# Performance work log

Hardware: AMD Instinct MI355X
Metric: run time of the kernel (lower is better)

## Reference

```python
import jax, jax.numpy as jnp
import numpy as np

N, E, F_IN = 50000, 1600000, 256
H, C = 4, 32            # heads, hidden_channels
HC = H * C
NUM_CLASSES = 16
NUM_GRAPHS = 64
NEG_SLOPE = 0.2


def setup_inputs() -> dict:
    key = jax.random.key(0)
    ks = jax.random.split(key, 16)
    x = jax.random.normal(ks[0], (N, F_IN), dtype=jnp.float32)
    edge_index = jax.random.randint(ks[1], (2, E), 0, N, dtype=jnp.int32)
    batch = jnp.sort(jax.random.randint(ks[2], (N,), 0, NUM_GRAPHS, dtype=jnp.int32))
    def glorot(k, shape):
        fan = shape[0] + shape[-1]
        return jax.random.uniform(k, shape, jnp.float32, -1.0, 1.0) * np.sqrt(6.0 / fan)
    return {
        "x": x, "edge_index": edge_index, "batch": batch,
        # GATConv 1
        "W1": glorot(ks[3], (F_IN, HC)),
        "att_src1": glorot(ks[4], (H, C)),
        "att_dst1": glorot(ks[5], (H, C)),
        "b1": jnp.zeros((HC,), jnp.float32),
        # GATConv 2
        "W2": glorot(ks[6], (HC, HC)),
        "att_src2": glorot(ks[7], (H, C)),
        "att_dst2": glorot(ks[8], (H, C)),
        "b2": jnp.zeros((HC,), jnp.float32),
        # classifier
        "Wc1": glorot(ks[9], (HC, C)),
        "bc1": jnp.zeros((C,), jnp.float32),
        "Wc2": glorot(ks[10], (C, NUM_CLASSES)),
        "bc2": jnp.zeros((NUM_CLASSES,), jnp.float32),
    }


def _gat_conv(x, src, dst, W, a_src, a_dst, b):
    # x: [N, F_in] -> h: [N, H, C]
    h = (x @ W).reshape(N, H, C)
    alpha_src = jnp.sum(h * a_src, axis=-1)   # [N, H]
    alpha_dst = jnp.sum(h * a_dst, axis=-1)   # [N, H]
    e = alpha_src[src] + alpha_dst[dst]       # [Etot, H]
    e = jax.nn.leaky_relu(e, NEG_SLOPE)
    # segment softmax over incoming edges of each dst node
    m = jax.ops.segment_max(e, dst, num_segments=N)          # [N, H]
    p = jnp.exp(e - m[dst])                                  # [Etot, H]
    z = jax.ops.segment_sum(p, dst, num_segments=N)          # [N, H]
    w = p / z[dst]
    out = jax.ops.segment_sum(h[src] * w[:, :, None], dst, num_segments=N)
    return out.reshape(N, HC) + b


def reference(x, edge_index, batch, W1, att_src1, att_dst1, b1,
              W2, att_src2, att_dst2, b2, Wc1, bc1, Wc2, bc2):
    # PyG GATConv default: add self-loops
    loop = jnp.arange(N, dtype=edge_index.dtype)
    src = jnp.concatenate([edge_index[0], loop])
    dst = jnp.concatenate([edge_index[1], loop])

    h = _gat_conv(x, src, dst, W1, att_src1, att_dst1, b1)
    h = jax.nn.relu(h)
    h = _gat_conv(h, src, dst, W2, att_src2, att_dst2, b2)
    h = jax.nn.relu(h)

    # global_mean_pool over batch ids
    sums = jax.ops.segment_sum(h, batch, num_segments=NUM_GRAPHS)      # [G, HC]
    cnts = jax.ops.segment_sum(jnp.ones((N, 1), h.dtype), batch, num_segments=NUM_GRAPHS)
    g = sums / cnts

    # classifier (dropout is identity in eval)
    g = g @ Wc1 + bc1
    g = g @ Wc2 + bc2
    return jax.nn.sigmoid(g)
```

## Files before the change

kernel.cpp:

```cpp
#include <hip/hip_runtime.h>
#include <math.h>

#define N_NODES 50000
#define E_EDGES 1600000
#define F_IN_DIM 256
#define H_HEADS 4
#define C_CH 32
#define HC 128
#define NUM_CLASSES 16
#define NUM_GRAPHS 64
#define ETOT (E_EDGES + N_NODES)
#define NEG_SLOPE 0.2f
#define SCAN_BLOCKS ((N_NODES + 255) / 256)
#define NBUCK ((N_NODES + 255) / 256)
#define SCAT_BLOCKS 512
#define POOL_SPLIT 8

__device__ __forceinline__ unsigned short f2bf(float f) {
    unsigned u = __float_as_uint(f);
    return (unsigned short)((u + 0x7FFFu + ((u >> 16) & 1u)) >> 16);
}

template <int K>
__global__ __launch_bounds__(256) void gemm_rb(const float* __restrict__ X,
                                               const float* __restrict__ W,
                                               float* __restrict__ Hout,
                                               unsigned short* __restrict__ H16) {
    __shared__ float xs[32][68];
    const int n0 = blockIdx.x * 64;
    const int tid = threadIdx.x;
    const int rg = tid >> 5;
    const int cg = tid & 31;
    const int r0 = rg * 8;
    const int c0 = cg * 4;
    float acc[8][4];
#pragma unroll
    for (int i = 0; i < 8; ++i)
#pragma unroll
        for (int j = 0; j < 4; ++j) acc[i][j] = 0.f;

    for (int k0 = 0; k0 < K; k0 += 32) {
        __syncthreads();
#pragma unroll
        for (int L = tid; L < 512; L += 256) {
            int row = L >> 3;
            int kq = L & 7;
            int n = n0 + row;
            float4 v = make_float4(0.f, 0.f, 0.f, 0.f);
            if (n < N_NODES)
                v = *reinterpret_cast<const float4*>(&X[(size_t)n * K + k0 + kq * 4]);
            xs[kq * 4 + 0][row] = v.x;
            xs[kq * 4 + 1][row] = v.y;
            xs[kq * 4 + 2][row] = v.z;
            xs[kq * 4 + 3][row] = v.w;
        }
        __syncthreads();
#pragma unroll 8
        for (int k = 0; k < 32; ++k) {
            const float4 w = *reinterpret_cast<const float4*>(&W[(size_t)(k0 + k) * HC + c0]);
            const float4 xa = *reinterpret_cast<const float4*>(&xs[k][r0]);
            const float4 xb = *reinterpret_cast<const float4*>(&xs[k][r0 + 4]);
            acc[0][0] = fmaf(xa.x, w.x, acc[0][0]);
            acc[0][1] = fmaf(xa.x, w.y, acc[0][1]);
            acc[0][2] = fmaf(xa.x, w.z, acc[0][2]);
            acc[0][3] = fmaf(xa.x, w.w, acc[0][3]);
            acc[1][0] = fmaf(xa.y, w.x, acc[1][0]);
            acc[1][1] = fmaf(xa.y, w.y, acc[1][1]);
            acc[1][2] = fmaf(xa.y, w.z, acc[1][2]);
            acc[1][3] = fmaf(xa.y, w.w, acc[1][3]);
            acc[2][0] = fmaf(xa.z, w.x, acc[2][0]);
            acc[2][1] = fmaf(xa.z, w.y, acc[2][1]);
            acc[2][2] = fmaf(xa.z, w.z, acc[2][2]);
            acc[2][3] = fmaf(xa.z, w.w, acc[2][3]);
            acc[3][0] = fmaf(xa.w, w.x, acc[3][0]);
            acc[3][1] = fmaf(xa.w, w.y, acc[3][1]);
            acc[3][2] = fmaf(xa.w, w.z, acc[3][2]);
            acc[3][3] = fmaf(xa.w, w.w, acc[3][3]);
            acc[4][0] = fmaf(xb.x, w.x, acc[4][0]);
            acc[4][1] = fmaf(xb.x, w.y, acc[4][1]);
            acc[4][2] = fmaf(xb.x, w.z, acc[4][2]);
            acc[4][3] = fmaf(xb.x, w.w, acc[4][3]);
            acc[5][0] = fmaf(xb.y, w.x, acc[5][0]);
            acc[5][1] = fmaf(xb.y, w.y, acc[5][1]);
            acc[5][2] = fmaf(xb.y, w.z, acc[5][2]);
            acc[5][3] = fmaf(xb.y, w.w, acc[5][3]);
            acc[6][0] = fmaf(xb.z, w.x, acc[6][0]);
            acc[6][1] = fmaf(xb.z, w.y, acc[6][1]);
            acc[6][2] = fmaf(xb.z, w.z, acc[6][2]);
            acc[6][3] = fmaf(xb.z, w.w, acc[6][3]);
            acc[7][0] = fmaf(xb.w, w.x, acc[7][0]);
            acc[7][1] = fmaf(xb.w, w.y, acc[7][1]);
            acc[7][2] = fmaf(xb.w, w.z, acc[7][2]);
            acc[7][3] = fmaf(xb.w, w.w, acc[7][3]);
        }
    }
#pragma unroll
    for (int i = 0; i < 8; ++i) {
        int n = n0 + r0 + i;
        if (n < N_NODES) {
            *reinterpret_cast<float4*>(&Hout[(size_t)n * HC + c0]) =
                make_float4(acc[i][0], acc[i][1], acc[i][2], acc[i][3]);
            ushort4 b;
            b.x = f2bf(acc[i][0]);
            b.y = f2bf(acc[i][1]);
            b.z = f2bf(acc[i][2]);
            b.w = f2bf(acc[i][3]);
            *reinterpret_cast<ushort4*>(&H16[(size_t)n * HC + c0]) = b;
        }
    }
}

__global__ void alpha_kernel(const float* __restrict__ Hb,
                             const float* __restrict__ a_src,
                             const float* __restrict__ a_dst,
                             float* __restrict__ as, float* __restrict__ ad) {
    int i = blockIdx.x * blockDim.x + threadIdx.x;
    if (i >= N_NODES * H_HEADS) return;
    int h = i & 3;
    const float* hp = Hb + (size_t)(i >> 2) * HC + h * C_CH;
    float ssum = 0.f, dsum = 0.f;
#pragma unroll
    for (int c = 0; c < C_CH; ++c) {
        float v = hp[c];
        ssum += v * a_src[h * C_CH + c];
        dsum += v * a_dst[h * C_CH + c];
    }
    as[i] = ssum;
    ad[i] = dsum;
}

__global__ void count_deg_kernel(const int* __restrict__ ei, int* __restrict__ deg) {
    int e = blockIdx.x * blockDim.x + threadIdx.x;
    if (e >= ETOT) return;
    int d = (e < E_EDGES) ? ei[E_EDGES + e] : (e - E_EDGES);
    atomicAdd(&deg[d], 1);
}

__global__ __launch_bounds__(256) void scan_block_kernel(const int* __restrict__ deg,
                                                         int* __restrict__ excl,
                                                         int* __restrict__ bsum) {
    __shared__ int tmp[256];
    int i = blockIdx.x * 256 + threadIdx.x;
    int v = (i < N_NODES) ? deg[i] : 0;
    tmp[threadIdx.x] = v;
    __syncthreads();
    for (int off = 1; off < 256; off <<= 1) {
        int t = (threadIdx.x >= off) ? tmp[threadIdx.x - off] : 0;
        __syncthreads();
        tmp[threadIdx.x] += t;
        __syncthreads();
    }
    if (i < N_NODES) excl[i] = tmp[threadIdx.x] - v;
    if (threadIdx.x == 255) bsum[blockIdx.x] = tmp[255];
}

__global__ __launch_bounds__(256) void scan_tops_kernel(int* __restrict__ bsum) {
    __shared__ int tmp[256];
    int t = threadIdx.x;
    int v = (t < SCAN_BLOCKS) ? bsum[t] : 0;
    tmp[t] = v;
    __syncthreads();
    for (int off = 1; off < 256; off <<= 1) {
        int u = (t >= off) ? tmp[t - off] : 0;
        __syncthreads();
        tmp[t] += u;
        __syncthreads();
    }
    if (t < SCAN_BLOCKS) bsum[t] = tmp[t] - v;
}

__global__ void scan_add_kernel(int* __restrict__ excl, const int* __restrict__ bsum,
                                int* __restrict__ bcursor) {
    int i = blockIdx.x * blockDim.x + threadIdx.x;
    if (i >= N_NODES) return;
    int s = excl[i] + bsum[i >> 8];
    excl[i] = s;
    if ((i & 255) == 0) bcursor[i >> 8] = s;
}

__global__ __launch_bounds__(256) void bucket_scatter_kernel(const int* __restrict__ ei,
                                                             int* __restrict__ bcursor,
                                                             unsigned* __restrict__ bucket_buf) {
    __shared__ int hist[NBUCK];
    __shared__ int base[NBUCK];
    const int tid = threadIdx.x;
    const int chunk = (ETOT + SCAT_BLOCKS - 1) / SCAT_BLOCKS;
    const int e0 = blockIdx.x * chunk;
    const int e1 = min(e0 + chunk, ETOT);
    for (int i = tid; i < NBUCK; i += 256) hist[i] = 0;
    __syncthreads();
    for (int e = e0 + tid; e < e1; e += 256) {
        int d = (e < E_EDGES) ? ei[E_EDGES + e] : (e - E_EDGES);
        atomicAdd(&hist[d >> 8], 1);
    }
    __syncthreads();
    for (int i = tid; i < NBUCK; i += 256) {
        int cnt = hist[i];
        base[i] = (cnt > 0) ? atomicAdd(&bcursor[i], cnt) : 0;
        hist[i] = 0;
    }
    __syncthreads();
    for (int e = e0 + tid; e < e1; e += 256) {
        int s, d;
        if (e < E_EDGES) { s = ei[e]; d = ei[E_EDGES + e]; }
        else             { s = d = e - E_EDGES; }
        int b = d >> 8;
        int pos = base[b] + atomicAdd(&hist[b], 1);
        bucket_buf[pos] = ((unsigned)d << 16) | (unsigned)s;
    }
}

__global__ __launch_bounds__(256) void bucket_sort_kernel(const unsigned* __restrict__ bucket_buf,
                                                          const int* __restrict__ row_start,
                                                          int* __restrict__ elist) {
    __shared__ int cur[256];
    const int b = blockIdx.x;
    const int n0 = b * 256;
    const int tid = threadIdx.x;
    if (n0 + tid < N_NODES) cur[tid] = row_start[n0 + tid];
    const int start = row_start[n0];
    const int end = (b == NBUCK - 1) ? ETOT : row_start[n0 + 256];
    __syncthreads();
    for (int j = start + tid; j < end; j += 256) {
        unsigned p = bucket_buf[j];
        int d = (int)(p >> 16);
        int s = (int)(p & 0xffffu);
        int pos = atomicAdd(&cur[d - n0], 1);
        elist[pos] = s;
    }
}

__global__ __launch_bounds__(128) void gat_gather_kernel(const int* __restrict__ row_start,
                                                         const int* __restrict__ deg,
                                                         const int* __restrict__ elist,
                                                         const float* __restrict__ as,
                                                         const float* __restrict__ ad,
                                                         const unsigned short* __restrict__ H16,
                                                         const float* __restrict__ bias,
                                                         float* __restrict__ out) {
    const int n = blockIdx.x;
    const int t = threadIdx.x;
    const int c = t;
    const int hg = t >> 5;
    const int j32 = t & 31;
    const int row = row_start[n];
    const int len = deg[n];
    const float ad_n = ad[n * 4 + hg];

    __shared__ int   sbuf[32];
    __shared__ float pbuf[4][32];

    float m = -INFINITY, z = 0.f, acc = 0.f;

    for (int base = 0; base < len; base += 32) {
        const int cl = min(32, len - base);
        if (t < cl) sbuf[t] = elist[row + base + t];
        __syncthreads();

        float ev = -INFINITY;
        if (j32 < cl) {
            int s = sbuf[j32];
            ev = as[s * 4 + hg] + ad_n;
            ev = ev > 0.f ? ev : ev * NEG_SLOPE;
        }
        float cm = ev;
#pragma unroll
        for (int off = 16; off > 0; off >>= 1)
            cm = fmaxf(cm, __shfl_xor(cm, off, 32));
        float mnew = fmaxf(m, cm);
        float scale = __expf(m - mnew);
        z *= scale;
        acc *= scale;
        m = mnew;
        float p = (j32 < cl) ? __expf(ev - m) : 0.f;
        float ps = p;
#pragma unroll
        for (int off = 16; off > 0; off >>= 1)
            ps += __shfl_xor(ps, off, 32);
        z += ps;
        pbuf[hg][j32] = p;
        __syncthreads();

        for (int j = 0; j < cl; ++j) {
            int s = sbuf[j];
            unsigned short us = H16[(size_t)s * HC + c];
            float hv = __uint_as_float((unsigned)us << 16);
            acc = fmaf(pbuf[hg][j], hv, acc);
        }
        __syncthreads();
    }
    float v = acc / z + bias[c];
    out[(size_t)n * HC + c] = v > 0.f ? v : 0.f;
}

__global__ void boundary_kernel(const int* __restrict__ batch,
                                int* __restrict__ gstart,
                                float* __restrict__ cntf) {
    int g = threadIdx.x;
    if (g <= NUM_GRAPHS) {
        int lo = 0, hi = N_NODES;
        while (lo < hi) {
            int mid = (lo + hi) >> 1;
            if (batch[mid] < g) lo = mid + 1; else hi = mid;
        }
        gstart[g] = lo;
    }
    __syncthreads();
    if (g < NUM_GRAPHS) cntf[g] = (float)(gstart[g + 1] - gstart[g]);
}

__global__ __launch_bounds__(128) void pool_seg_kernel(const float* __restrict__ out,
                                                       const int* __restrict__ gstart,
                                                       float* __restrict__ sums) {
    const int g = blockIdx.x >> 3;
    const int split = blockIdx.x & 7;
    const int c = threadIdx.x;
    const int start = gstart[g], end = gstart[g + 1];
    const int len = end - start;
    const int chunk = (len + POOL_SPLIT - 1) / POOL_SPLIT;
    const int s0 = start + split * chunk;
    const int s1 = min(s0 + chunk, end);
    float acc = 0.f;
    for (int n = s0; n < s1; ++n) acc += out[(size_t)n * HC + c];
    if (s0 < s1) atomicAdd(&sums[g * HC + c], acc);
}

__global__ void classifier_kernel(const float* __restrict__ sums,
                                  const float* __restrict__ cnt,
                                  const float* __restrict__ Wc1,
                                  const float* __restrict__ bc1,
                                  const float* __restrict__ Wc2,
                                  const float* __restrict__ bc2,
                                  float* __restrict__ outp) {
    int g = threadIdx.x;
    if (g >= NUM_GRAPHS) return;
    float inv = 1.0f / cnt[g];
    float hidden[C_CH];
#pragma unroll 4
    for (int j = 0; j < C_CH; ++j) {
        float acc = bc1[j];
        for (int c = 0; c < HC; ++c)
            acc += (sums[g * HC + c] * inv) * Wc1[c * C_CH + j];
        hidden[j] = acc;
    }
    for (int k = 0; k < NUM_CLASSES; ++k) {
        float acc = bc2[k];
#pragma unroll
        for (int j = 0; j < C_CH; ++j) acc += hidden[j] * Wc2[j * NUM_CLASSES + k];
        outp[g * NUM_CLASSES + k] = 1.0f / (1.0f + __expf(-acc));
    }
}

extern "C" void kernel_launch(void* const* d_in, const int* in_sizes, int n_in,
                              void* d_out, int out_size, void* d_ws, size_t ws_size,
                              hipStream_t stream) {
    const float* x   = (const float*)d_in[0];
    const int*   ei  = (const int*)  d_in[1];
    const int*   bat = (const int*)  d_in[2];
    const float* W1  = (const float*)d_in[3];
    const float* as1 = (const float*)d_in[4];
    const float* ad1 = (const float*)d_in[5];
    const float* b1  = (const float*)d_in[6];
    const float* W2  = (const float*)d_in[7];
    const float* as2 = (const float*)d_in[8];
    const float* ad2 = (const float*)d_in[9];
    const float* b2  = (const float*)d_in[10];
    const float* Wc1 = (const float*)d_in[11];
    const float* bc1 = (const float*)d_in[12];
    const float* Wc2 = (const float*)d_in[13];
    const float* bc2 = (const float*)d_in[14];
    float* outp = (float*)d_out;

    char* ws = (char*)d_ws;
    float* hbuf = (float*)ws;  ws += (size_t)N_NODES * HC * 4;
    float* obuf = (float*)ws;  ws += (size_t)N_NODES * HC * 4;
    unsigned short* hb16 = (unsigned short*)ws; ws += (size_t)N_NODES * HC * 2;
    float* asb  = (float*)ws;  ws += (size_t)N_NODES * H_HEADS * 4;
    float* adb  = (float*)ws;  ws += (size_t)N_NODES * H_HEADS * 4;
    int* elist    = (int*)ws;  ws += (size_t)ETOT * 4;
    unsigned* bucket_buf = (unsigned*)ws; ws += (size_t)ETOT * 4;
    int* row_start= (int*)ws;  ws += (size_t)N_NODES * 4;
    int* degb     = (int*)ws;  ws += (size_t)N_NODES * 4;
    int* bcursor  = (int*)ws;  ws += (size_t)NBUCK * 4;
    int* bsum     = (int*)ws;  ws += 256 * 4;
    int* gstart   = (int*)ws;  ws += (NUM_GRAPHS + 1) * 4;
    float* sums = (float*)ws;  ws += (size_t)NUM_GRAPHS * HC * 4;
    float* cnt  = (float*)ws;  ws += (size_t)NUM_GRAPHS * 4;

    const int nh_blocks  = (N_NODES * H_HEADS + 255) / 256;
    const int n_blocks   = (N_NODES + 255) / 256;
    const int e_blocks   = (ETOT + 255) / 256;
    const int gemm_blocks = (N_NODES + 63) / 64;

    hipMemsetAsync(degb, 0, (size_t)N_NODES * 4, stream);
    count_deg_kernel<<<e_blocks, 256, 0, stream>>>(ei, degb);
    scan_block_kernel<<<SCAN_BLOCKS, 256, 0, stream>>>(degb, row_start, bsum);
    scan_tops_kernel<<<1, 256, 0, stream>>>(bsum);
    scan_add_kernel<<<n_blocks, 256, 0, stream>>>(row_start, bsum, bcursor);
    bucket_scatter_kernel<<<SCAT_BLOCKS, 256, 0, stream>>>(ei, bcursor, bucket_buf);
    bucket_sort_kernel<<<NBUCK, 256, 0, stream>>>(bucket_buf, row_start, elist);

    gemm_rb<F_IN_DIM><<<gemm_blocks, 256, 0, stream>>>(x, W1, hbuf, hb16);
    alpha_kernel<<<nh_blocks, 256, 0, stream>>>(hbuf, as1, ad1, asb, adb);
    gat_gather_kernel<<<N_NODES, 128, 0, stream>>>(row_start, degb, elist,
                                                   asb, adb, hb16, b1, obuf);

    gemm_rb<HC><<<gemm_blocks, 256, 0, stream>>>(obuf, W2, hbuf, hb16);
    alpha_kernel<<<nh_blocks, 256, 0, stream>>>(hbuf, as2, ad2, asb, adb);
    gat_gather_kernel<<<N_NODES, 128, 0, stream>>>(row_start, degb, elist,
                                                   asb, adb, hb16, b2, obuf);

    boundary_kernel<<<1, 128, 0, stream>>>(bat, gstart, cnt);
    hipMemsetAsync(sums, 0, (size_t)NUM_GRAPHS * HC * 4, stream);
    pool_seg_kernel<<<NUM_GRAPHS * POOL_SPLIT, 128, 0, stream>>>(obuf, gstart, sums);
    classifier_kernel<<<1, 64, 0, stream>>>(sums, cnt, Wc1, bc1, Wc2, bc2, outp);
}
```

Measured before the change: 637.9 us.

## Fuse attention scores into GEMM epilogue and gather one node per wavefront

The attention-coefficient computation moves into the GEMM epilogue, using shuffle reductions across the 8 lanes that cover one head. This removes the separate alpha kernel and the fp32 H buffer write and read-back. The gather kernel now gives each node one 64-lane wavefront instead of a 128-thread block. Each lane handles two channels through a packed bf16 load, and edge indices and weights are broadcast by shuffles instead of shared memory, which removes the block barriers. Chunks shrink to 16 edges per head group, so there are more iterations of online softmax rescaling.

```diff
diff --git a/kernel.cpp b/kernel.cpp
--- a/kernel.cpp
+++ b/kernel.cpp
@@ -24,8 +24,11 @@
 template <int K>
 __global__ __launch_bounds__(256) void gemm_rb(const float* __restrict__ X,
                                                const float* __restrict__ W,
-                                               float* __restrict__ Hout,
-                                               unsigned short* __restrict__ H16) {
+                                               const float* __restrict__ att_src,
+                                               const float* __restrict__ att_dst,
+                                               unsigned short* __restrict__ H16,
+                                               float* __restrict__ as,
+                                               float* __restrict__ ad) {
     __shared__ float xs[32][68];
     const int n0 = blockIdx.x * 64;
     const int tid = threadIdx.x;
@@ -94,39 +97,33 @@
             acc[7][3] = fmaf(xb.w, w.w, acc[7][3]);
         }
     }
+    const int h = cg >> 3;
+    const int cb = c0 & 31;
+    const float4 av = *reinterpret_cast<const float4*>(&att_src[h * C_CH + cb]);
+    const float4 dv = *reinterpret_cast<const float4*>(&att_dst[h * C_CH + cb]);
 #pragma unroll
     for (int i = 0; i < 8; ++i) {
         int n = n0 + r0 + i;
+        float sa = acc[i][0] * av.x + acc[i][1] * av.y + acc[i][2] * av.z + acc[i][3] * av.w;
+        float sd = acc[i][0] * dv.x + acc[i][1] * dv.y + acc[i][2] * dv.z + acc[i][3] * dv.w;
+#pragma unroll
+        for (int off = 1; off < 8; off <<= 1) {
+            sa += __shfl_xor(sa, off, 64);
+            sd += __shfl_xor(sd, off, 64);
+        }
         if (n < N_NODES) {
-            *reinterpret_cast<float4*>(&Hout[(size_t)n * HC + c0]) =
-                make_float4(acc[i][0], acc[i][1], acc[i][2], acc[i][3]);
             ushort4 b;
             b.x = f2bf(acc[i][0]);
             b.y = f2bf(acc[i][1]);
             b.z = f2bf(acc[i][2]);
             b.w = f2bf(acc[i][3]);
             *reinterpret_cast<ushort4*>(&H16[(size_t)n * HC + c0]) = b;
-        }
-    }
-}
-
-__global__ void alpha_kernel(const float* __restrict__ Hb,
-                             const float* __restrict__ a_src,
-                             const float* __restrict__ a_dst,
-                             float* __restrict__ as, float* __restrict__ ad) {
-    int i = blockIdx.x * blockDim.x + threadIdx.x;
-    if (i >= N_NODES * H_HEADS) return;
-    int h = i & 3;
-    const float* hp = Hb + (size_t)(i >> 2) * HC + h * C_CH;
-    float ssum = 0.f, dsum = 0.f;
-#pragma unroll
-    for (int c = 0; c < C_CH; ++c) {
-        float v = hp[c];
-        ssum += v * a_src[h * C_CH + c];
-        dsum += v * a_dst[h * C_CH + c];
-    }
-    as[i] = ssum;
-    ad[i] = dsum;
+            if ((cg & 7) == 0) {
+                as[n * 4 + h] = sa;
+                ad[n * 4 + h] = sd;
+            }
+        }
+    }
 }
 
 __global__ void count_deg_kernel(const int* __restrict__ ei, int* __restrict__ deg) {
@@ -230,7 +227,7 @@
     }
 }
 
-__global__ __launch_bounds__(128) void gat_gather_kernel(const int* __restrict__ row_start,
+__global__ __launch_bounds__(256) void gat_gather_kernel(const int* __restrict__ row_start,
                                                          const int* __restrict__ deg,
                                                          const int* __restrict__ elist,
                                                          const float* __restrict__ as,
@@ -238,59 +235,61 @@
                                                          const unsigned short* __restrict__ H16,
                                                          const float* __restrict__ bias,
                                                          float* __restrict__ out) {
-    const int n = blockIdx.x;
-    const int t = threadIdx.x;
-    const int c = t;
-    const int hg = t >> 5;
-    const int j32 = t & 31;
+    const int n = blockIdx.x * 4 + (threadIdx.x >> 6);
+    if (n >= N_NODES) return;
+    const int lane = threadIdx.x & 63;
+    const int hg = lane >> 4;
+    const int j16 = lane & 15;
     const int row = row_start[n];
     const int len = deg[n];
     const float ad_n = ad[n * 4 + hg];
 
-    __shared__ int   sbuf[32];
-    __shared__ float pbuf[4][32];
-
-    float m = -INFINITY, z = 0.f, acc = 0.f;
-
-    for (int base = 0; base < len; base += 32) {
-        const int cl = min(32, len - base);
-        if (t < cl) sbuf[t] = elist[row + base + t];
-        __syncthreads();
+    float m = -INFINITY, z = 0.f, acc0 = 0.f, acc1 = 0.f;
+
+    for (int base = 0; base < len; base += 16) {
+        const int cl = min(16, len - base);
+        int sval = (j16 < cl) ? elist[row + base + j16] : 0;
 
         float ev = -INFINITY;
-        if (j32 < cl) {
-            int s = sbuf[j32];
-            ev = as[s * 4 + hg] + ad_n;
+        if (j16 < cl) {
+            ev = as[sval * 4 + hg] + ad_n;
             ev = ev > 0.f ? ev : ev * NEG_SLOPE;
         }
         float cm = ev;
 #pragma unroll
-        for (int off = 16; off > 0; off >>= 1)
-            cm = fmaxf(cm, __shfl_xor(cm, off, 32));
+        for (int off = 8; off > 0; off >>= 1)
+            cm = fmaxf(cm, __shfl_xor(cm, off, 64));
         float mnew = fmaxf(m, cm);
         float scale = __expf(m - mnew);
         z *= scale;
-        acc *= scale;
+        acc0 *= scale;
+        acc1 *= scale;
         m = mnew;
-        float p = (j32 < cl) ? __expf(ev - m) : 0.f;
+        float p = (j16 < cl) ? __expf(ev - m) : 0.f;
         float ps = p;
 #pragma unroll
-        for (int off = 16; off > 0; off >>= 1)
-            ps += __shfl_xor(ps, off, 32);
+        for (int off = 8; off > 0; off >>= 1)
+            ps += __shfl_xor(ps, off, 64);
         z += ps;
-        pbuf[hg][j32] = p;
-        __syncthreads();
 
         for (int j = 0; j < cl; ++j) {
-            int s = sbuf[j];
-            unsigned short us = H16[(size_t)s * HC + c];
-            float hv = __uint_as_float((unsigned)us << 16);
-            acc = fmaf(pbuf[hg][j], hv, acc);
-        }
-        __syncthreads();
-    }
-    float v = acc / z + bias[c];
-    out[(size_t)n * HC + c] = v > 0.f ? v : 0.f;
+            int src = (lane & 48) | j;
+            int sj = __shfl(sval, src, 64);
+            float pj = __shfl(p, src, 64);
+            unsigned u = *reinterpret_cast<const unsigned*>(&H16[(size_t)sj * HC + 2 * lane]);
+            float hv0 = __uint_as_float(u << 16);
+            float hv1 = __uint_as_float(u & 0xffff0000u);
+            acc0 = fmaf(pj, hv0, acc0);
+            acc1 = fmaf(pj, hv1, acc1);
+        }
+    }
+    float inv = 1.0f / z;
+    float v0 = acc0 * inv + bias[2 * lane];
+    float v1 = acc1 * inv + bias[2 * lane + 1];
+    float2 r;
+    r.x = v0 > 0.f ? v0 : 0.f;
+    r.y = v1 > 0.f ? v1 : 0.f;
+    *reinterpret_cast<float2*>(&out[(size_t)n * HC + 2 * lane]) = r;
 }
 
 __global__ void boundary_kernel(const int* __restrict__ batch,
@@ -372,7 +371,6 @@
     float* outp = (float*)d_out;
 
     char* ws = (char*)d_ws;
-    float* hbuf = (float*)ws;  ws += (size_t)N_NODES * HC * 4;
     float* obuf = (float*)ws;  ws += (size_t)N_NODES * HC * 4;
     unsigned short* hb16 = (unsigned short*)ws; ws += (size_t)N_NODES * HC * 2;
     float* asb  = (float*)ws;  ws += (size_t)N_NODES * H_HEADS * 4;
@@ -387,10 +385,10 @@
     float* sums = (float*)ws;  ws += (size_t)NUM_GRAPHS * HC * 4;
     float* cnt  = (float*)ws;  ws += (size_t)NUM_GRAPHS * 4;
 
-    const int nh_blocks  = (N_NODES * H_HEADS + 255) / 256;
     const int n_blocks   = (N_NODES + 255) / 256;
     const int e_blocks   = (ETOT + 255) / 256;
     const int gemm_blocks = (N_NODES + 63) / 64;
+    const int gat_blocks  = (N_NODES + 3) / 4;
 
     hipMemsetAsync(degb, 0, (size_t)N_NODES * 4, stream);
     count_deg_kernel<<<e_blocks, 256, 0, stream>>>(ei, degb);
@@ -400,15 +398,13 @@
     bucket_scatter_kernel<<<SCAT_BLOCKS, 256, 0, stream>>>(ei, bcursor, bucket_buf);
     bucket_sort_kernel<<<NBUCK, 256, 0, stream>>>(bucket_buf, row_start, elist);
 
-    gemm_rb<F_IN_DIM><<<gemm_blocks, 256, 0, stream>>>(x, W1, hbuf, hb16);
-    alpha_kernel<<<nh_blocks, 256, 0, stream>>>(hbuf, as1, ad1, asb, adb);
-    gat_gather_kernel<<<N_NODES, 128, 0, stream>>>(row_start, degb, elist,
-                                                   asb, adb, hb16, b1, obuf);
-
-    gemm_rb<HC><<<gemm_blocks, 256, 0, stream>>>(obuf, W2, hbuf, hb16);
-    alpha_kernel<<<nh_blocks, 256, 0, stream>>>(hbuf, as2, ad2, asb, adb);
-    gat_gather_kernel<<<N_NODES, 128, 0, stream>>>(row_start, degb, elist,
-                                                   asb, adb, hb16, b2, obuf);
+    gemm_rb<F_IN_DIM><<<gemm_blocks, 256, 0, stream>>>(x, W1, as1, ad1, hb16, asb, adb);
+    gat_gather_kernel<<<gat_blocks, 256, 0, stream>>>(row_start, degb, elist,
+                                                      asb, adb, hb16, b1, obuf);
+
+    gemm_rb<HC><<<gemm_blocks, 256, 0, stream>>>(obuf, W2, as2, ad2, hb16, asb, adb);
+    gat_gather_kernel<<<gat_blocks, 256, 0, stream>>>(row_start, degb, elist,
+                                                      asb, adb, hb16, b2, obuf);
 
     boundary_kernel<<<1, 128, 0, stream>>>(bat, gstart, cnt);
     hipMemsetAsync(sums, 0, (size_t)NUM_GRAPHS * HC * 4, stream);
```

Measured after the change: 693.4 us. 1.09x slower.
